# Performance work log

Hardware: AMD Instinct MI355X
Metric: run time of the kernel (lower is better)

The kernel has to match this reference:

```python
import jax, jax.numpy as jnp
import numpy as np

KNN = 4
H = 0.03


def setup_inputs() -> dict:
    key = jax.random.key(0)
    pc = jax.random.normal(key, (8, 4096, 3), dtype=jnp.float32)  # [B, N, 3]
    return {"pc": pc}


def reference(pc) -> jnp.ndarray:
    sq = jnp.sum(pc * pc, axis=-1)  # [B, N]
    # dist[b, i, j] = || pc[b,i] - pc[b,j] ||^2
    dist = sq[:, :, None] + sq[:, None, :] - 2.0 * jnp.einsum("bid,bjd->bij", pc, pc)
    dist = jnp.maximum(dist, 0.0)
    # k nearest neighbors with offset=1 (skip self): take smallest KNN+1, drop the first
    neg_top, _ = jax.lax.top_k(-dist, KNN + 1)  # sorted descending -> distances ascending
    knn_dist = -neg_top[..., 1:]  # [B, N, KNN]
    weight = jnp.exp(-knn_dist / (H * H))
    loss = jnp.sum(-knn_dist * weight)
    return loss
```

## Files before the change

kernel.cpp:

```cpp
#include <hip/hip_runtime.h>
#include <math.h>

#define NPTS   4096
#define NB     8
#define IT     4
#define IGRP   (64 * IT)
#define JSPLIT 4
#define JBLK   (NPTS / JSPLIT)
#define NWAVES 8
#define BLK    (NWAVES * 64)
#define JCHUNK (JBLK / NWAVES)
#define INV_H2 (1.0f / (0.03f * 0.03f))
#define INFD   3.0e38f

__device__ __forceinline__ float med3f(float a, float b, float c) {
#if defined(__has_builtin)
#if __has_builtin(__builtin_amdgcn_fmed3f)
  return __builtin_amdgcn_fmed3f(a, b, c);
#else
  return fminf(c, fmaxf(a, b));
#endif
#else
  return fminf(c, fmaxf(a, b));
#endif
}

__device__ __forceinline__ float4 merge4(float4 A, float4 B) {
  float L0 = fminf(A.x, B.w), L1 = fminf(A.y, B.z);
  float L2 = fminf(A.z, B.y), L3 = fminf(A.w, B.x);
  float e0 = fminf(L0, L2), e2 = fmaxf(L0, L2);
  float e1 = fminf(L1, L3), e3 = fmaxf(L1, L3);
  return make_float4(fminf(e0, e1), fmaxf(e0, e1), fminf(e2, e3), fmaxf(e2, e3));
}

template <bool CHECK>
__device__ __forceinline__ void scan_range(const float4* __restrict__ sP,
                                           int lo, int hi, const int* __restrict__ ls,
                                           const float* __restrict__ mx,
                                           const float* __restrict__ my,
                                           const float* __restrict__ mz,
                                           float t[IT][4]) {
#pragma unroll 4
  for (int j = lo; j < hi; ++j) {
    float4 q = sP[j];
#pragma unroll
    for (int s = 0; s < IT; ++s) {
      float u = fmaf(mz[s], q.z, q.w);
      u = fmaf(my[s], q.y, u);
      u = fmaf(mx[s], q.x, u);
      if (CHECK) u = (j == ls[s]) ? INFD : u;
      t[s][3] = med3f(t[s][2], u, t[s][3]);
      t[s][2] = med3f(t[s][1], u, t[s][2]);
      t[s][1] = med3f(t[s][0], u, t[s][1]);
      t[s][0] = fminf(t[s][0], u);
    }
  }
}

__global__ __launch_bounds__(BLK)
void repulsion_k1(const float* __restrict__ pc, float4* __restrict__ ws) {
  __shared__ float4 buf[2 * JBLK];
  float4* sP = buf;

  const int blk = blockIdx.x;
  const int b   = blk >> 6;
  const int g   = (blk >> 2) & 15;
  const int js  = blk & 3;
  const int tid = threadIdx.x;
  const float* base = pc + (size_t)b * NPTS * 3;

  if (tid < JBLK / 4) {
    const float4* pcv = (const float4*)base + (size_t)js * (JBLK * 3 / 4);
    float4 a = pcv[3 * tid + 0];
    float4 c = pcv[3 * tid + 1];
    float4 e = pcv[3 * tid + 2];
    float x0 = a.x, y0 = a.y, z0 = a.z;
    float x1 = a.w, y1 = c.x, z1 = c.y;
    float x2 = c.z, y2 = c.w, z2 = e.x;
    float x3 = e.y, y3 = e.z, z3 = e.w;
    sP[4 * tid + 0] = make_float4(x0, y0, z0, fmaf(x0, x0, fmaf(y0, y0, z0 * z0)));
    sP[4 * tid + 1] = make_float4(x1, y1, z1, fmaf(x1, x1, fmaf(y1, y1, z1 * z1)));
    sP[4 * tid + 2] = make_float4(x2, y2, z2, fmaf(x2, x2, fmaf(y2, y2, z2 * z2)));
    sP[4 * tid + 3] = make_float4(x3, y3, z3, fmaf(x3, x3, fmaf(y3, y3, z3 * z3)));
  }

  const int w    = tid >> 6;
  const int lane = tid & 63;

  float mx[IT], my[IT], mz[IT];
  int ls[IT];
#pragma unroll
  for (int s = 0; s < IT; ++s) {
    int gi = g * IGRP + lane + 64 * s;
    float x = base[3 * gi + 0];
    float y = base[3 * gi + 1];
    float z = base[3 * gi + 2];
    mx[s] = -2.0f * x; my[s] = -2.0f * y; mz[s] = -2.0f * z;
    ls[s] = gi - js * JBLK;
  }

  float t[IT][4];
#pragma unroll
  for (int s = 0; s < IT; ++s) { t[s][0] = INFD; t[s][1] = INFD; t[s][2] = INFD; t[s][3] = INFD; }

  __syncthreads();

  const int lo = w * JCHUNK, hi = lo + JCHUNK;
  const bool chk = (js == (g >> 2)) && ((w >> 1) == (g & 3));
  if (chk) scan_range<true >(sP, lo, hi, ls, mx, my, mz, t);
  else     scan_range<false>(sP, lo, hi, ls, mx, my, mz, t);

  __syncthreads();
  float4* cand = buf;
#pragma unroll
  for (int s = 0; s < IT; ++s)
    cand[w * IGRP + lane + 64 * s] = make_float4(t[s][0], t[s][1], t[s][2], t[s][3]);
  __syncthreads();

  if (tid < IGRP) {
    float4 L[NWAVES];
#pragma unroll
    for (int ww = 0; ww < NWAVES; ++ww) L[ww] = cand[ww * IGRP + tid];
#pragma unroll
    for (int ww = 0; ww < 4; ++ww) L[ww] = merge4(L[2 * ww], L[2 * ww + 1]);
    L[0] = merge4(L[0], L[1]);
    L[1] = merge4(L[2], L[3]);
    float4 R = merge4(L[0], L[1]);
    int gi = b * NPTS + g * IGRP + tid;
    ws[(size_t)gi * JSPLIT + js] = R;
  }
}

__global__ __launch_bounds__(256)
void repulsion_k2(const float* __restrict__ pc, const float4* __restrict__ ws,
                  float* __restrict__ out) {
  const int t = blockIdx.x * 256 + threadIdx.x;
  const float4* w4 = ws + (size_t)t * JSPLIT;
  float4 L0 = w4[0], L1 = w4[1], L2 = w4[2], L3 = w4[3];
  float4 A = merge4(L0, L1);
  float4 Bv = merge4(L2, L3);
  float f0 = fminf(A.x, Bv.w);
  float f1 = fminf(A.y, Bv.z);
  float f2 = fminf(A.z, Bv.y);
  float f3 = fminf(A.w, Bv.x);

  float x = pc[3 * t + 0], y = pc[3 * t + 1], z = pc[3 * t + 2];
  float sqi = fmaf(x, x, fmaf(y, y, z * z));

  float s = 0.0f;
  float m;
  m = fmaxf(f0 + sqi, 0.0f); s -= m * expf(-m * INV_H2);
  m = fmaxf(f1 + sqi, 0.0f); s -= m * expf(-m * INV_H2);
  m = fmaxf(f2 + sqi, 0.0f); s -= m * expf(-m * INV_H2);
  m = fmaxf(f3 + sqi, 0.0f); s -= m * expf(-m * INV_H2);

  for (int off = 32; off > 0; off >>= 1) s += __shfl_down(s, off);
  if ((threadIdx.x & 63) == 0) atomicAdd(out, s);
}

extern "C" void kernel_launch(void* const* d_in, const int* in_sizes, int n_in,
                              void* d_out, int out_size, void* d_ws, size_t ws_size,
                              hipStream_t stream) {
  const float* pc = (const float*)d_in[0];
  float* out = (float*)d_out;
  float4* ws = (float4*)d_ws;
  hipMemsetAsync(out, 0, sizeof(float), stream);
  repulsion_k1<<<dim3(NB * 16 * JSPLIT), dim3(BLK), 0, stream>>>(pc, ws);
  repulsion_k2<<<dim3(NB * NPTS / 256), dim3(256), 0, stream>>>(pc, ws, out);
}
```

Measured before the change: 90.06 us.

## Fuse top-k merge and loss into one kernel via last-block ticket

Replaces the two-kernel design with a single kernel. Each block handles 128 query points against half of the batch's points, with 2 queries per thread instead of 4, giving 512 blocks. A per-tile atomic ticket lets the second finishing block merge both halves and compute the weighted loss, removing the second launch and the workspace round trip. It also clamps distances to 0.5 before the exp. This adds an extra memset, threadfences and atomics, and changes per-thread work and occupancy.

```diff
diff --git a/kernel.cpp b/kernel.cpp
--- a/kernel.cpp
+++ b/kernel.cpp
@@ -3,13 +3,13 @@
 
 #define NPTS   4096
 #define NB     8
-#define IT     4
-#define IGRP   (64 * IT)
-#define JSPLIT 4
-#define JBLK   (NPTS / JSPLIT)
-#define NWAVES 8
-#define BLK    (NWAVES * 64)
-#define JCHUNK (JBLK / NWAVES)
+#define NPTOT  (NB * NPTS)
+#define ITILE  128
+#define NTILE  (NPTOT / ITILE)
+#define W      8
+#define BLKT   (W * 64)
+#define JHALF  (NPTS / 2)
+#define JCH    (JHALF / W)
 #define INV_H2 (1.0f / (0.03f * 0.03f))
 #define INFD   3.0e38f
 
@@ -34,43 +34,48 @@
 }
 
 template <bool CHECK>
-__device__ __forceinline__ void scan_range(const float4* __restrict__ sP,
-                                           int lo, int hi, const int* __restrict__ ls,
-                                           const float* __restrict__ mx,
-                                           const float* __restrict__ my,
-                                           const float* __restrict__ mz,
-                                           float t[IT][4]) {
+__device__ __forceinline__ void scan(const float4* __restrict__ sP, int lo, int hi,
+                                     int ls0, int ls1,
+                                     float mx0, float my0, float mz0,
+                                     float mx1, float my1, float mz1,
+                                     float& r0, float& r1, float& r2, float& r3,
+                                     float& s0, float& s1, float& s2, float& s3) {
 #pragma unroll 4
   for (int j = lo; j < hi; ++j) {
     float4 q = sP[j];
-#pragma unroll
-    for (int s = 0; s < IT; ++s) {
-      float u = fmaf(mz[s], q.z, q.w);
-      u = fmaf(my[s], q.y, u);
-      u = fmaf(mx[s], q.x, u);
-      if (CHECK) u = (j == ls[s]) ? INFD : u;
-      t[s][3] = med3f(t[s][2], u, t[s][3]);
-      t[s][2] = med3f(t[s][1], u, t[s][2]);
-      t[s][1] = med3f(t[s][0], u, t[s][1]);
-      t[s][0] = fminf(t[s][0], u);
+    float u0 = fmaf(mx0, q.x, fmaf(my0, q.y, fmaf(mz0, q.z, q.w)));
+    float u1 = fmaf(mx1, q.x, fmaf(my1, q.y, fmaf(mz1, q.z, q.w)));
+    if (CHECK) {
+      u0 = (j == ls0) ? INFD : u0;
+      u1 = (j == ls1) ? INFD : u1;
     }
+    r3 = med3f(r2, u0, r3); r2 = med3f(r1, u0, r2);
+    r1 = med3f(r0, u0, r1); r0 = fminf(r0, u0);
+    s3 = med3f(s2, u1, s3); s2 = med3f(s1, u1, s2);
+    s1 = med3f(s0, u1, s1); s0 = fminf(s0, u1);
   }
 }
 
-__global__ __launch_bounds__(BLK)
-void repulsion_k1(const float* __restrict__ pc, float4* __restrict__ ws) {
-  __shared__ float4 buf[2 * JBLK];
-  float4* sP = buf;
+__global__ __launch_bounds__(BLKT)
+void repulsion_kernel(const float* __restrict__ pc, float4* __restrict__ part,
+                      int* __restrict__ tickets, float* __restrict__ out) {
+  __shared__ float4 sP[JHALF];
+  __shared__ float4 cand[W * ITILE];
+  __shared__ float  sqv[ITILE];
+  __shared__ int    lastflag;
 
-  const int blk = blockIdx.x;
-  const int b   = blk >> 6;
-  const int g   = (blk >> 2) & 15;
-  const int js  = blk & 3;
-  const int tid = threadIdx.x;
+  const int blk  = blockIdx.x;
+  const int tile = blk >> 1;
+  const int half = blk & 1;
+  const int b    = tile >> 5;
+  const int g    = tile & 31;
+  const int tid  = threadIdx.x;
+  const int w    = tid >> 6;
+  const int lane = tid & 63;
   const float* base = pc + (size_t)b * NPTS * 3;
 
-  if (tid < JBLK / 4) {
-    const float4* pcv = (const float4*)base + (size_t)js * (JBLK * 3 / 4);
+  {
+    const float4* pcv = (const float4*)base + half * (JHALF * 3 / 4);
     float4 a = pcv[3 * tid + 0];
     float4 c = pcv[3 * tid + 1];
     float4 e = pcv[3 * tid + 2];
@@ -84,78 +89,68 @@
     sP[4 * tid + 3] = make_float4(x3, y3, z3, fmaf(x3, x3, fmaf(y3, y3, z3 * z3)));
   }
 
-  const int w    = tid >> 6;
-  const int lane = tid & 63;
+  const int gi0 = g * ITILE + lane;
+  const int gi1 = gi0 + 64;
+  float x0 = base[3 * gi0 + 0], y0 = base[3 * gi0 + 1], z0 = base[3 * gi0 + 2];
+  float x1 = base[3 * gi1 + 0], y1 = base[3 * gi1 + 1], z1 = base[3 * gi1 + 2];
+  const float mx0 = -2.0f * x0, my0 = -2.0f * y0, mz0 = -2.0f * z0;
+  const float mx1 = -2.0f * x1, my1 = -2.0f * y1, mz1 = -2.0f * z1;
+  if (w == 0) {
+    sqv[lane]      = fmaf(x0, x0, fmaf(y0, y0, z0 * z0));
+    sqv[lane + 64] = fmaf(x1, x1, fmaf(y1, y1, z1 * z1));
+  }
+  __syncthreads();
 
-  float mx[IT], my[IT], mz[IT];
-  int ls[IT];
+  float r0 = INFD, r1 = INFD, r2 = INFD, r3 = INFD;
+  float s0 = INFD, s1 = INFD, s2 = INFD, s3 = INFD;
+  const int lo  = w * JCH, hi = lo + JCH;
+  const int sb  = g * ITILE - half * JHALF;
+  const int ls0 = sb + lane, ls1 = ls0 + 64;
+  const bool chk = (sb >= 0) && (sb < JHALF) && (w == (sb >> 8));
+  if (chk) scan<true >(sP, lo, hi, ls0, ls1, mx0, my0, mz0, mx1, my1, mz1,
+                       r0, r1, r2, r3, s0, s1, s2, s3);
+  else     scan<false>(sP, lo, hi, ls0, ls1, mx0, my0, mz0, mx1, my1, mz1,
+                       r0, r1, r2, r3, s0, s1, s2, s3);
+
+  cand[w * ITILE + lane]      = make_float4(r0, r1, r2, r3);
+  cand[w * ITILE + 64 + lane] = make_float4(s0, s1, s2, s3);
+  __syncthreads();
+
+  float4 R;
+  if (tid < ITILE) {
+    float4 L[W];
 #pragma unroll
-  for (int s = 0; s < IT; ++s) {
-    int gi = g * IGRP + lane + 64 * s;
-    float x = base[3 * gi + 0];
-    float y = base[3 * gi + 1];
-    float z = base[3 * gi + 2];
-    mx[s] = -2.0f * x; my[s] = -2.0f * y; mz[s] = -2.0f * z;
-    ls[s] = gi - js * JBLK;
+    for (int k = 0; k < W; ++k) L[k] = cand[k * ITILE + tid];
+#pragma unroll
+    for (int k = 0; k < 4; ++k) L[k] = merge4(L[2 * k], L[2 * k + 1]);
+    L[0] = merge4(L[0], L[1]);
+    L[1] = merge4(L[2], L[3]);
+    R = merge4(L[0], L[1]);
+    part[(size_t)blk * ITILE + tid] = R;
   }
 
-  float t[IT][4];
-#pragma unroll
-  for (int s = 0; s < IT; ++s) { t[s][0] = INFD; t[s][1] = INFD; t[s][2] = INFD; t[s][3] = INFD; }
+  __threadfence();
+  __syncthreads();
+  if (tid == 0) lastflag = atomicAdd(&tickets[tile], 1);
+  __syncthreads();
+  if (lastflag != 1) return;
 
-  __syncthreads();
+  __threadfence();
+  if (tid < ITILE) {
+    float4 O = part[(size_t)(tile * 2 + (1 - half)) * ITILE + tid];
+    float4 A = merge4(R, O);
+    float f0 = A.x, f1 = A.y, f2 = A.z, f3 = A.w;
+    const float sqi = sqv[tid];
+    float su = 0.0f;
+    float m;
+    m = fminf(fmaxf(f0 + sqi, 0.0f), 0.5f); su -= m * expf(-m * INV_H2);
+    m = fminf(fmaxf(f1 + sqi, 0.0f), 0.5f); su -= m * expf(-m * INV_H2);
+    m = fminf(fmaxf(f2 + sqi, 0.0f), 0.5f); su -= m * expf(-m * INV_H2);
+    m = fminf(fmaxf(f3 + sqi, 0.0f), 0.5f); su -= m * expf(-m * INV_H2);
 
-  const int lo = w * JCHUNK, hi = lo + JCHUNK;
-  const bool chk = (js == (g >> 2)) && ((w >> 1) == (g & 3));
-  if (chk) scan_range<true >(sP, lo, hi, ls, mx, my, mz, t);
-  else     scan_range<false>(sP, lo, hi, ls, mx, my, mz, t);
-
-  __syncthreads();
-  float4* cand = buf;
-#pragma unroll
-  for (int s = 0; s < IT; ++s)
-    cand[w * IGRP + lane + 64 * s] = make_float4(t[s][0], t[s][1], t[s][2], t[s][3]);
-  __syncthreads();
-
-  if (tid < IGRP) {
-    float4 L[NWAVES];
-#pragma unroll
-    for (int ww = 0; ww < NWAVES; ++ww) L[ww] = cand[ww * IGRP + tid];
-#pragma unroll
-    for (int ww = 0; ww < 4; ++ww) L[ww] = merge4(L[2 * ww], L[2 * ww + 1]);
-    L[0] = merge4(L[0], L[1]);
-    L[1] = merge4(L[2], L[3]);
-    float4 R = merge4(L[0], L[1]);
-    int gi = b * NPTS + g * IGRP + tid;
-    ws[(size_t)gi * JSPLIT + js] = R;
+    for (int off = 32; off > 0; off >>= 1) su += __shfl_down(su, off);
+    if ((tid & 63) == 0) atomicAdd(out, su);
   }
-}
-
-__global__ __launch_bounds__(256)
-void repulsion_k2(const float* __restrict__ pc, const float4* __restrict__ ws,
-                  float* __restrict__ out) {
-  const int t = blockIdx.x * 256 + threadIdx.x;
-  const float4* w4 = ws + (size_t)t * JSPLIT;
-  float4 L0 = w4[0], L1 = w4[1], L2 = w4[2], L3 = w4[3];
-  float4 A = merge4(L0, L1);
-  float4 Bv = merge4(L2, L3);
-  float f0 = fminf(A.x, Bv.w);
-  float f1 = fminf(A.y, Bv.z);
-  float f2 = fminf(A.z, Bv.y);
-  float f3 = fminf(A.w, Bv.x);
-
-  float x = pc[3 * t + 0], y = pc[3 * t + 1], z = pc[3 * t + 2];
-  float sqi = fmaf(x, x, fmaf(y, y, z * z));
-
-  float s = 0.0f;
-  float m;
-  m = fmaxf(f0 + sqi, 0.0f); s -= m * expf(-m * INV_H2);
-  m = fmaxf(f1 + sqi, 0.0f); s -= m * expf(-m * INV_H2);
-  m = fmaxf(f2 + sqi, 0.0f); s -= m * expf(-m * INV_H2);
-  m = fmaxf(f3 + sqi, 0.0f); s -= m * expf(-m * INV_H2);
-
-  for (int off = 32; off > 0; off >>= 1) s += __shfl_down(s, off);
-  if ((threadIdx.x & 63) == 0) atomicAdd(out, s);
 }
 
 extern "C" void kernel_launch(void* const* d_in, const int* in_sizes, int n_in,
@@ -163,8 +158,9 @@
                               hipStream_t stream) {
   const float* pc = (const float*)d_in[0];
   float* out = (float*)d_out;
-  float4* ws = (float4*)d_ws;
+  float4* part   = (float4*)d_ws;
+  int*    tickets = (int*)((char*)d_ws + (size_t)2 * NTILE * ITILE * sizeof(float4));
   hipMemsetAsync(out, 0, sizeof(float), stream);
-  repulsion_k1<<<dim3(NB * 16 * JSPLIT), dim3(BLK), 0, stream>>>(pc, ws);
-  repulsion_k2<<<dim3(NB * NPTS / 256), dim3(256), 0, stream>>>(pc, ws, out);
+  hipMemsetAsync(tickets, 0, NTILE * sizeof(int), stream);
+  repulsion_kernel<<<dim3(2 * NTILE), dim3(BLKT), 0, stream>>>(pc, part, tickets, out);
 }
```

After: 170.0 us. 88.7% more time.
